# Kernel optimization log

Hardware: AMD Instinct MI355X
Metric: run time of the kernel (lower is better)

## Reference

```python
import jax, jax.numpy as jnp
import numpy as np

HIDDEN = 2048
NH = 32        # query heads
NKV = 4        # kv heads (GQA)
HD = 64        # head_dim
Q_SIZE = NH * HD      # 2048
KV_SIZE = NKV * HD    # 256
WINDOW = 1024         # sliding window size
THETA = 1000000.0
T = 2048              # tokens
SCALE = HD ** -0.5
NEG = -1e30


def setup_inputs() -> dict:
    key = jax.random.key(0)
    k1, k2, k3 = jax.random.split(key, 3)
    return {
        "positions": jnp.arange(T, dtype=jnp.int32),
        "hidden_states": jax.random.normal(k1, (T, HIDDEN), dtype=jnp.float32),
        "wqkv": jax.random.normal(k2, (HIDDEN, Q_SIZE + 2 * KV_SIZE), dtype=jnp.float32) * (HIDDEN ** -0.5),
        "wo": jax.random.normal(k3, (Q_SIZE, HIDDEN), dtype=jnp.float32) * (Q_SIZE ** -0.5),
    }


def _apply_rope(x, positions):
    # NeoX-style rotary embedding over full head_dim (rotate halves).
    half = HD // 2
    inv_freq = 1.0 / (THETA ** (jnp.arange(half, dtype=jnp.float32) / half))
    ang = positions.astype(jnp.float32)[:, None] * inv_freq[None, :]   # [T, half]
    cos = jnp.cos(ang)[:, None, :]   # [T, 1, half]
    sin = jnp.sin(ang)[:, None, :]
    x1, x2 = jnp.split(x, 2, axis=-1)
    return jnp.concatenate([x1 * cos - x2 * sin, x2 * cos + x1 * sin], axis=-1)


def reference(positions, hidden_states, wqkv, wo):
    # fused QKV projection
    qkv = hidden_states @ wqkv                          # [T, Q+2KV]
    q = qkv[:, :Q_SIZE].reshape(T, NH, HD)
    k = qkv[:, Q_SIZE:Q_SIZE + KV_SIZE].reshape(T, NKV, HD)
    v = qkv[:, Q_SIZE + KV_SIZE:].reshape(T, NKV, HD)
    # rotary embedding on q, k
    q = _apply_rope(q, positions)
    k = _apply_rope(k, positions)
    # GQA: repeat kv heads to match query heads
    group = NH // NKV
    kr = jnp.repeat(k, group, axis=1)                   # [T, NH, HD]
    vr = jnp.repeat(v, group, axis=1)
    scores = jnp.einsum('qhd,khd->hqk', q, kr) * SCALE  # [NH, T, T]
    # causal + sliding-window mask: attend to j in (i-WINDOW, i]
    i = jnp.arange(T)[:, None]
    j = jnp.arange(T)[None, :]
    mask = (j <= i) & (i - j < WINDOW)                  # [T, T]
    scores = jnp.where(mask[None, :, :], scores, NEG)
    probs = jax.nn.softmax(scores, axis=-1)
    attn = jnp.einsum('hqk,khd->qhd', probs, vr).reshape(T, Q_SIZE)
    return attn @ wo                                    # [T, HIDDEN]
```

## Files before the change

### kernel.cpp

```cpp
#include <hip/hip_runtime.h>
#include <hip/hip_bf16.h>

typedef float  f32x4  __attribute__((ext_vector_type(4)));
typedef __bf16 bf16x8 __attribute__((ext_vector_type(8)));
typedef __bf16 bf16x4 __attribute__((ext_vector_type(4)));
typedef __bf16 bf16x2 __attribute__((ext_vector_type(2)));

#define T_SEQ   2048
#define HIDDEN  2048
#define NH      32
#define NKV     4
#define HD      64
#define QSZ     2048
#define KVSZ    256
#define QKVN    2560
#define WINDOW  1024

#if __has_builtin(__builtin_amdgcn_exp2f)
#define EXPS(x) __builtin_amdgcn_exp2f(x)
#define QSCALE  0.1803368801111f
#else
#define EXPS(x) __expf(x)
#define QSCALE  0.125f
#endif

#define RAW_BARRIER()   asm volatile("s_barrier" ::: "memory")
#define WAITV(n)        asm volatile("s_waitcnt vmcnt(" #n ")" ::: "memory")

__device__ __forceinline__ void gll16(const __bf16* g, __bf16* l) {
    __builtin_amdgcn_global_load_lds(
        (const __attribute__((address_space(1))) void*)g,
        (__attribute__((address_space(3))) void*)l,
        16, 0, 0);
}

__global__ __launch_bounds__(256) void prep(const float4* __restrict__ hidden4,
                                            bf16x4* __restrict__ hidden_bf4,
                                            const float* __restrict__ wqkv,
                                            const float* __restrict__ wo,
                                            __bf16* __restrict__ wqkv_t,
                                            __bf16* __restrict__ wo_t,
                                            const int* __restrict__ pos,
                                            float2* __restrict__ ropetab) {
    __shared__ float tile[32][132];
    const int b = blockIdx.x;
    const int tid = threadIdx.x;

    if (b < 4096) {
        int id = b * 256 + tid;
        float4 v = hidden4[id];
        bf16x4 o;
        o[0] = (__bf16)v.x; o[1] = (__bf16)v.y; o[2] = (__bf16)v.z; o[3] = (__bf16)v.w;
        hidden_bf4[id] = o;
        return;
    }
    if (b < 4352) {
        int id = (b - 4096) * 256 + tid;
        int row = id >> 5, f = id & 31;
        float p = (float)pos[row];
        float ifr = exp2f((float)f * -0.62286151779138f);
        float sn, cs;
        sincosf(p * ifr, &sn, &cs);
        ropetab[id] = make_float2(cs, sn);
        return;
    }

    const float* in;
    __bf16* out;
    int Rin, Cin, bx, by;
    if (b < 5632) {
        int t = b - 4352;
        in = wqkv; out = wqkv_t; Rin = 2048; Cin = 2560;
        bx = t % 20; by = t / 20;
    } else {
        int t = b - 5632;
        in = wo; out = wo_t; Rin = 2048; Cin = 2048;
        bx = t % 16; by = t / 16;
    }
    const int ri = by * 32, ci = bx * 128;
    const int r0 = tid >> 5;
    const int c4 = tid & 31;
    #pragma unroll
    for (int i = 0; i < 4; i++) {
        float4 v = *reinterpret_cast<const float4*>(
            &in[(size_t)(ri + r0 + i * 8) * Cin + ci + c4 * 4]);
        *reinterpret_cast<float4*>(&tile[r0 + i * 8][c4 * 4]) = v;
    }
    __syncthreads();
    const int c  = tid >> 3;
    const int rb = tid & 7;
    #pragma unroll
    for (int j = 0; j < 4; j++) {
        int cc = c + j * 32;
        bf16x4 pk;
        #pragma unroll
        for (int i = 0; i < 4; i++) pk[i] = (__bf16)tile[rb * 4 + i][cc];
        *reinterpret_cast<bf16x4*>(&out[(size_t)(ci + cc) * Rin + ri + rb * 4]) = pk;
    }
}


#define GEMM_PROLOGUE(Aptr, Btptr, Kdim)                                        \
    __shared__ __align__(16) __bf16 Asm[2][64 * 64];                            \
    __shared__ __align__(16) __bf16 Bsm[2][128 * 64];                           \
    const int tid = threadIdx.x;                                                \
    const int wid = tid >> 6;                                                   \
    const int l   = tid & 63;                                                   \
    const int lg  = l >> 4;                                                     \
    const int ll  = l & 15;                                                     \
    const int swl = ll & 7;                                                     \
    const int wm  = wid >> 1, wn = wid & 1;                                     \
    const int gx   = gridDim.x;                                                 \
    const int flat = blockIdx.y * gx + blockIdx.x;                              \
    const int nwg  = gx * gridDim.y;                                            \
    const int swz  = (flat & 7) * (nwg >> 3) + (flat >> 3);                     \
    const int bm   = (swz / gx) * 64;                                           \
    const int bn   = (swz % gx) * 128;                                          \
    const __bf16* Ab = (Aptr) + (size_t)bm * (Kdim);                            \
    const __bf16* Bb = (Btptr) + (size_t)bn * (Kdim);                           \
    f32x4 acc[2][4];                                                            \
    _Pragma("unroll")                                                           \
    for (int i = 0; i < 2; i++)                                                 \
        _Pragma("unroll")                                                       \
        for (int j = 0; j < 4; j++)                                             \
            acc[i][j] = (f32x4){0.f, 0.f, 0.f, 0.f};                            \
    const int srow = tid >> 3;                                                  \
    const int sseg0 = tid & 7;

#define GEMM_STAGE(buf, k0, Kdim)                                               \
    {                                                                           \
        _Pragma("unroll")                                                       \
        for (int c = 0; c < 2; c++) {                                           \
            int row  = c * 32 + srow;                                           \
            int sseg = sseg0 ^ (row & 7);                                       \
            gll16(Ab + (size_t)row * (Kdim) + (k0) + sseg * 8,                  \
                  &Asm[buf][(c * 256 + tid) * 8]);                              \
        }                                                                       \
        _Pragma("unroll")                                                       \
        for (int c = 0; c < 4; c++) {                                           \
            int row  = c * 32 + srow;                                           \
            int sseg = sseg0 ^ (row & 7);                                       \
            gll16(Bb + (size_t)row * (Kdim) + (k0) + sseg * 8,                  \
                  &Bsm[buf][(c * 256 + tid) * 8]);                              \
        }                                                                       \
    }

#define GEMM_KLOOP(Kdim)                                                        \
    GEMM_STAGE(0, 0, Kdim)                                                      \
    int cur = 0;                                                                \
    for (int k0 = 0; k0 < (Kdim); k0 += 64) {                                   \
        RAW_BARRIER();               \
        if (k0 + 64 < (Kdim)) {                                                 \
            GEMM_STAGE(cur ^ 1, k0 + 64, Kdim)                                  \
            WAITV(6);                 \
        } else {                                                                \
            WAITV(0);                                                           \
        }                                                                       \
        RAW_BARRIER();                             \
        __builtin_amdgcn_sched_barrier(0);                                      \
        _Pragma("unroll")                                                       \
        for (int ss = 0; ss < 2; ss++) {                                        \
            bf16x8 af[2], bfr[4];                                               \
            _Pragma("unroll")                                                   \
            for (int mi = 0; mi < 2; mi++) {                                    \
                int r = wm * 32 + mi * 16 + ll;                                 \
                int u = (ss * 4 + lg) ^ swl;                                    \
                af[mi] = *reinterpret_cast<const bf16x8*>(&Asm[cur][r * 64 + u * 8]); \
            }                                                                   \
            _Pragma("unroll")                                                   \
            for (int ni = 0; ni < 4; ni++) {                                    \
                int r = wn * 64 + ni * 16 + ll;                                 \
                int u = (ss * 4 + lg) ^ swl;                                    \
                bfr[ni] = *reinterpret_cast<const bf16x8*>(&Bsm[cur][r * 64 + u * 8]); \
            }                                                                   \
            _Pragma("unroll")                                                   \
            for (int mi = 0; mi < 2; mi++)                                      \
                _Pragma("unroll")                                               \
                for (int ni = 0; ni < 4; ni++)                                  \
                    acc[mi][ni] = __builtin_amdgcn_mfma_f32_16x16x32_bf16(      \
                        af[mi], bfr[ni], acc[mi][ni], 0, 0, 0);                 \
        }                                                                       \
        cur ^= 1;                                                               \
    }

__global__ __launch_bounds__(256) void gemm_out(const __bf16* __restrict__ A,
                                                const __bf16* __restrict__ Bt,
                                                float* __restrict__ Cout,
                                                int M, int N, int K) {
    GEMM_PROLOGUE(A, Bt, K)
    GEMM_KLOOP(K)
    #pragma unroll
    for (int mi = 0; mi < 2; mi++)
        #pragma unroll
        for (int ni = 0; ni < 4; ni++)
            #pragma unroll
            for (int r = 0; r < 4; r++) {
                int row = bm + wm*32 + mi*16 + lg*4 + r;
                int col = bn + wn*64 + ni*16 + ll;
                Cout[(size_t)row * N + col] = acc[mi][ni][r];
            }
}

__global__ __launch_bounds__(256) void gemm_qkv(const __bf16* __restrict__ A,
                                                const __bf16* __restrict__ Bt,
                                                const float2* __restrict__ ropetab,
                                                __bf16* __restrict__ q,
                                                __bf16* __restrict__ k,
                                                __bf16* __restrict__ vT) {
    GEMM_PROLOGUE(A, Bt, HIDDEN)
    GEMM_KLOOP(HIDDEN)

    if (bn < QSZ + KVSZ) {
        const bool isq = (bn < QSZ);
        #pragma unroll
        for (int mi = 0; mi < 2; mi++) {
            #pragma unroll
            for (int r = 0; r < 4; r++) {
                int row = bm + wm*32 + mi*16 + lg*4 + r;
                const float2* tb = &ropetab[row * 32 + ll];
                #pragma unroll
                for (int ni = 0; ni < 2; ni++) {
                    float2 cssn = tb[ni * 16];
                    float x1 = acc[mi][ni][r], x2 = acc[mi][ni + 2][r];
                    float o1 = x1 * cssn.x - x2 * cssn.y;
                    float o2 = x2 * cssn.x + x1 * cssn.y;
                    int col = bn + wn*64 + ni*16 + ll;
                    if (isq) {
                        q[(size_t)row * QSZ + col]      = (__bf16)(o1 * QSCALE);
                        q[(size_t)row * QSZ + col + 32] = (__bf16)(o2 * QSCALE);
                    } else {
                        k[(size_t)row * KVSZ + (col - QSZ)]      = (__bf16)o1;
                        k[(size_t)row * KVSZ + (col - QSZ) + 32] = (__bf16)o2;
                    }
                }
            }
        }
    } else {
        #pragma unroll
        for (int mi = 0; mi < 2; mi++) {
            int row0 = bm + wm*32 + mi*16 + lg*4;
            #pragma unroll
            for (int ni = 0; ni < 4; ni++) {
                int d = bn + wn*64 + ni*16 + ll - (QSZ + KVSZ);
                bf16x4 pk;
                #pragma unroll
                for (int r = 0; r < 4; r++) pk[r] = (__bf16)acc[mi][ni][r];
                *reinterpret_cast<bf16x4*>(&vT[(size_t)d * T_SEQ + row0]) = pk;
            }
        }
    }
}

__global__ __launch_bounds__(512) void attn_kernel(const __bf16* __restrict__ qg,
                                                   const __bf16* __restrict__ kgl,
                                                   const __bf16* __restrict__ vTg,
                                                   __bf16* __restrict__ og) {
    const int qb  = blockIdx.x;
    const int hp  = blockIdx.y;
    const int kvh = hp >> 2;
    const int tid = threadIdx.x;
    const int wid = tid >> 6;
    const int h   = hp * 2 + (wid >> 2);
    const int l   = tid & 63;
    const int lg  = l >> 4;
    const int ll  = l & 15;
    const int i0  = qb * 64;
    const int qw  = i0 + (wid & 3) * 16;
    const int qi  = qw + ll;

    __shared__ __align__(16) __bf16 Ksm[2][64 * 64];
    __shared__ __align__(16) __bf16 VTs[2][64 * 64];

    bf16x8 qf[2];
    {
        const __bf16* qp = qg + (size_t)(qw + ll) * QSZ + h * 64 + lg * 8;
        qf[0] = *reinterpret_cast<const bf16x8*>(qp);
        qf[1] = *reinterpret_cast<const bf16x8*>(qp + 32);
    }

    f32x4 o[4];
    #pragma unroll
    for (int dn = 0; dn < 4; dn++) o[dn] = (f32x4){0.f, 0.f, 0.f, 0.f};
    float l_run = 0.f;

    int jlo = i0 - (WINDOW - 1); if (jlo < 0) jlo = 0;
    int t0v = jlo & ~63;
    int tend = i0 + 64;

    const int srow = tid >> 3;
    const int sg   = (tid & 7) ^ (srow & 7);
    const int krow = (srow & 35) | ((srow & 8) << 1) | ((srow & 4) << 1) | ((srow & 16) >> 2);
    const __bf16* kp = kgl + (size_t)krow * KVSZ + kvh * 64 + sg * 8;
    const __bf16* vp = vTg + (size_t)(kvh * 64 + srow) * T_SEQ + sg * 8;

#define ASTAGE(buf, t)                                      \
    {                                                       \
        gll16(kp + (size_t)(t) * KVSZ, &Ksm[buf][tid * 8]); \
        gll16(vp + (t),                &VTs[buf][tid * 8]); \
    }

    ASTAGE(0, t0v);

    const int swl = ll & 7;
    const int u0 = (lg ^ swl) * 8;
    const int u1 = ((4 + lg) ^ swl) * 8;

    int cur = 0;
    for (int t = t0v; t < tend; t += 64) {
        RAW_BARRIER();
        if (t + 64 < tend) {
            ASTAGE(cur ^ 1, t + 64);
            WAITV(2);
        } else {
            WAITV(0);
        }
        RAW_BARRIER();
        __builtin_amdgcn_sched_barrier(0);

        bool active = (t <= qw + 15) && (t + 63 >= qw - (WINDOW - 1));
        if (active) {
            f32x4 sT[4];
            __builtin_amdgcn_s_setprio(1);
            #pragma unroll
            for (int kt = 0; kt < 4; kt++) {
                sT[kt] = (f32x4){0.f, 0.f, 0.f, 0.f};
                bf16x8 kf0 = *reinterpret_cast<const bf16x8*>(&Ksm[cur][kt*1024 + ll*64 + u0]);
                sT[kt] = __builtin_amdgcn_mfma_f32_16x16x32_bf16(kf0, qf[0], sT[kt], 0, 0, 0);
                bf16x8 kf1 = *reinterpret_cast<const bf16x8*>(&Ksm[cur][kt*1024 + ll*64 + u1]);
                sT[kt] = __builtin_amdgcn_mfma_f32_16x16x32_bf16(kf1, qf[1], sT[kt], 0, 0, 0);
            }
            __builtin_amdgcn_s_setprio(0);

            bool full = (t + 63 <= qw) && (t >= qw + 15 - (WINDOW - 1));
            float ts = 0.f;
            if (full) {
                #pragma unroll
                for (int kt = 0; kt < 4; kt++) {
                    #pragma unroll
                    for (int r = 0; r < 4; r++) {
                        float p = EXPS(sT[kt][r]);
                        sT[kt][r] = p;
                        ts += p;
                    }
                }
            } else {
                #pragma unroll
                for (int kt = 0; kt < 4; kt++) {
                    int jb = t + ((kt & 2) << 4) + ((kt & 1) << 2) + (lg << 3);
                    #pragma unroll
                    for (int r = 0; r < 4; r++) {
                        int j = jb + r;
                        bool ok = (j <= qi) && (qi - j < WINDOW);
                        float p = ok ? EXPS(sT[kt][r]) : 0.f;
                        sT[kt][r] = p;
                        ts += p;
                    }
                }
            }
            ts += __shfl_xor(ts, 16);
            ts += __shfl_xor(ts, 32);
            l_run += ts;

            __builtin_amdgcn_s_setprio(1);
            #pragma unroll
            for (int kt2 = 0; kt2 < 2; kt2++) {
                bf16x8 pa;
                #pragma unroll
                for (int r = 0; r < 4; r++) {
                    pa[r]     = (__bf16)sT[kt2*2][r];
                    pa[r + 4] = (__bf16)sT[kt2*2 + 1][r];
                }
                int uv = kt2 ? u1 : u0;
                #pragma unroll
                for (int dn = 0; dn < 4; dn++) {
                    bf16x8 vf = *reinterpret_cast<const bf16x8*>(&VTs[cur][dn*1024 + ll*64 + uv]);
                    o[dn] = __builtin_amdgcn_mfma_f32_16x16x32_bf16(pa, vf, o[dn], 0, 0, 0);
                }
            }
            __builtin_amdgcn_s_setprio(0);
        }
        cur ^= 1;
    }
#undef ASTAGE

    float linv = 1.0f / l_run;
    float i0v = __shfl(linv, lg*4 + 0);
    float i1v = __shfl(linv, lg*4 + 1);
    float i2v = __shfl(linv, lg*4 + 2);
    float i3v = __shfl(linv, lg*4 + 3);
    #pragma unroll
    for (int dn = 0; dn < 4; dn++) {
        og[(size_t)(qw + lg*4 + 0) * QSZ + h*64 + dn*16 + ll] = (__bf16)(o[dn][0] * i0v);
        og[(size_t)(qw + lg*4 + 1) * QSZ + h*64 + dn*16 + ll] = (__bf16)(o[dn][1] * i1v);
        og[(size_t)(qw + lg*4 + 2) * QSZ + h*64 + dn*16 + ll] = (__bf16)(o[dn][2] * i2v);
        og[(size_t)(qw + lg*4 + 3) * QSZ + h*64 + dn*16 + ll] = (__bf16)(o[dn][3] * i3v);
    }
}

extern "C" void kernel_launch(void* const* d_in, const int* in_sizes, int n_in,
                              void* d_out, int out_size, void* d_ws, size_t ws_size,
                              hipStream_t stream) {
    const int*   positions = (const int*)d_in[0];
    const float* hidden    = (const float*)d_in[1];
    const float* wqkv      = (const float*)d_in[2];
    const float* wo        = (const float*)d_in[3];
    float* out = (float*)d_out;

    char* ws = (char*)d_ws;
    __bf16* hidden_bf = (__bf16*)(ws);
    __bf16* wqkv_t    = (__bf16*)(ws + 8388608);
    __bf16* wo_t      = (__bf16*)(ws + 18874368);
    __bf16* q_bf      = (__bf16*)(ws + 37748736);
    __bf16* k_bf      = (__bf16*)(ws + 46137344);
    __bf16* vT_bf     = (__bf16*)(ws + 47185920);
    __bf16* attn_bf   = (__bf16*)(ws + 48234496);
    float2* ropetab   = (float2*)(ws + 56623104);

    prep<<<dim3(6656), dim3(256), 0, stream>>>(
        (const float4*)hidden, (bf16x4*)hidden_bf, wqkv, wo,
        wqkv_t, wo_t, positions, ropetab);

    gemm_qkv<<<dim3(QKVN / 128, T_SEQ / 64), dim3(256), 0, stream>>>(
        hidden_bf, wqkv_t, ropetab, q_bf, k_bf, vT_bf);

    attn_kernel<<<dim3(T_SEQ / 64, 16), dim3(512), 0, stream>>>(
        q_bf, k_bf, vT_bf, attn_bf);

    gemm_out<<<dim3(HIDDEN / 128, T_SEQ / 64), dim3(256), 0, stream>>>(
        attn_bf, wo_t, out, T_SEQ, HIDDEN, QSZ);
}
```

Measured before the change: 106.7 us.

## Use triple-buffered LDS pipeline in output GEMM and attention kernels

Switches the output-projection GEMM and the attention K/V loop from double to triple buffering. Loads run two tiles ahead and are issued after the single per-iteration barrier, which removes one barrier per iteration. The aim is to hide more global-load latency. The cost is 50% more LDS per block in both kernels, which may reduce occupancy.

```diff
diff --git a/kernel.cpp b/kernel.cpp
--- a/kernel.cpp
+++ b/kernel.cpp
@@ -100,9 +100,7 @@
 }
 
 
-#define GEMM_PROLOGUE(Aptr, Btptr, Kdim)                                        \
-    __shared__ __align__(16) __bf16 Asm[2][64 * 64];                            \
-    __shared__ __align__(16) __bf16 Bsm[2][128 * 64];                           \
+#define GEMM_PROLOGUE_COMMON(Aptr, Btptr, Kdim)                                 \
     const int tid = threadIdx.x;                                                \
     const int wid = tid >> 6;                                                   \
     const int l   = tid & 63;                                                   \
@@ -145,50 +143,71 @@
         }                                                                       \
     }
 
-#define GEMM_KLOOP(Kdim)                                                        \
+#define GEMM_COMPUTE(bufidx)                                                    \
+    _Pragma("unroll")                                                           \
+    for (int ss = 0; ss < 2; ss++) {                                            \
+        bf16x8 af[2], bfr[4];                                                   \
+        _Pragma("unroll")                                                       \
+        for (int mi = 0; mi < 2; mi++) {                                        \
+            int r = wm * 32 + mi * 16 + ll;                                     \
+            int u = (ss * 4 + lg) ^ swl;                                        \
+            af[mi] = *reinterpret_cast<const bf16x8*>(&Asm[bufidx][r * 64 + u * 8]); \
+        }                                                                       \
+        _Pragma("unroll")                                                       \
+        for (int ni = 0; ni < 4; ni++) {                                        \
+            int r = wn * 64 + ni * 16 + ll;                                     \
+            int u = (ss * 4 + lg) ^ swl;                                        \
+            bfr[ni] = *reinterpret_cast<const bf16x8*>(&Bsm[bufidx][r * 64 + u * 8]); \
+        }                                                                       \
+        _Pragma("unroll")                                                       \
+        for (int mi = 0; mi < 2; mi++)                                          \
+            _Pragma("unroll")                                                   \
+            for (int ni = 0; ni < 4; ni++)                                      \
+                acc[mi][ni] = __builtin_amdgcn_mfma_f32_16x16x32_bf16(          \
+                    af[mi], bfr[ni], acc[mi][ni], 0, 0, 0);                     \
+    }
+
+#define GEMM_KLOOP2(Kdim)                                                       \
     GEMM_STAGE(0, 0, Kdim)                                                      \
     int cur = 0;                                                                \
     for (int k0 = 0; k0 < (Kdim); k0 += 64) {                                   \
-        RAW_BARRIER();               \
+        RAW_BARRIER();                                                          \
         if (k0 + 64 < (Kdim)) {                                                 \
             GEMM_STAGE(cur ^ 1, k0 + 64, Kdim)                                  \
-            WAITV(6);                 \
+            WAITV(6);                                                           \
         } else {                                                                \
             WAITV(0);                                                           \
         }                                                                       \
-        RAW_BARRIER();                             \
+        RAW_BARRIER();                                                          \
         __builtin_amdgcn_sched_barrier(0);                                      \
-        _Pragma("unroll")                                                       \
-        for (int ss = 0; ss < 2; ss++) {                                        \
-            bf16x8 af[2], bfr[4];                                               \
-            _Pragma("unroll")                                                   \
-            for (int mi = 0; mi < 2; mi++) {                                    \
-                int r = wm * 32 + mi * 16 + ll;                                 \
-                int u = (ss * 4 + lg) ^ swl;                                    \
-                af[mi] = *reinterpret_cast<const bf16x8*>(&Asm[cur][r * 64 + u * 8]); \
-            }                                                                   \
-            _Pragma("unroll")                                                   \
-            for (int ni = 0; ni < 4; ni++) {                                    \
-                int r = wn * 64 + ni * 16 + ll;                                 \
-                int u = (ss * 4 + lg) ^ swl;                                    \
-                bfr[ni] = *reinterpret_cast<const bf16x8*>(&Bsm[cur][r * 64 + u * 8]); \
-            }                                                                   \
-            _Pragma("unroll")                                                   \
-            for (int mi = 0; mi < 2; mi++)                                      \
-                _Pragma("unroll")                                               \
-                for (int ni = 0; ni < 4; ni++)                                  \
-                    acc[mi][ni] = __builtin_amdgcn_mfma_f32_16x16x32_bf16(      \
-                        af[mi], bfr[ni], acc[mi][ni], 0, 0, 0);                 \
-        }                                                                       \
+        GEMM_COMPUTE(cur)                                                       \
         cur ^= 1;                                                               \
+    }
+
+#define GEMM_KLOOP3(Kdim)                                                       \
+    GEMM_STAGE(0, 0, Kdim)                                                      \
+    GEMM_STAGE(1, 64, Kdim)                                                     \
+    int cur = 0;                                                                \
+    for (int k0 = 0; k0 < (Kdim); k0 += 64) {                                   \
+        if (k0 + 64 < (Kdim)) { WAITV(6); } else { WAITV(0); }                  \
+        RAW_BARRIER();                                                          \
+        __builtin_amdgcn_sched_barrier(0);                                      \
+        if (k0 + 128 < (Kdim)) {                                                \
+            int nb = cur + 2; if (nb >= 3) nb -= 3;                             \
+            GEMM_STAGE(nb, k0 + 128, Kdim)                                      \
+        }                                                                       \
+        GEMM_COMPUTE(cur)                                                       \
+        cur = (cur == 2) ? 0 : cur + 1;                                         \
     }
 
 __global__ __launch_bounds__(256) void gemm_out(const __bf16* __restrict__ A,
                                                 const __bf16* __restrict__ Bt,
                                                 float* __restrict__ Cout,
                                                 int M, int N, int K) {
-    GEMM_PROLOGUE(A, Bt, K)
-    GEMM_KLOOP(K)
+    __shared__ __align__(16) __bf16 Asm[3][64 * 64];
+    __shared__ __align__(16) __bf16 Bsm[3][128 * 64];
+    GEMM_PROLOGUE_COMMON(A, Bt, K)
+    GEMM_KLOOP3(K)
     #pragma unroll
     for (int mi = 0; mi < 2; mi++)
         #pragma unroll
@@ -207,8 +226,10 @@
                                                 __bf16* __restrict__ q,
                                                 __bf16* __restrict__ k,
                                                 __bf16* __restrict__ vT) {
-    GEMM_PROLOGUE(A, Bt, HIDDEN)
-    GEMM_KLOOP(HIDDEN)
+    __shared__ __align__(16) __bf16 Asm[2][64 * 64];
+    __shared__ __align__(16) __bf16 Bsm[2][128 * 64];
+    GEMM_PROLOGUE_COMMON(A, Bt, HIDDEN)
+    GEMM_KLOOP2(HIDDEN)
 
     if (bn < QSZ + KVSZ) {
         const bool isq = (bn < QSZ);
@@ -268,8 +289,8 @@
     const int qw  = i0 + (wid & 3) * 16;
     const int qi  = qw + ll;
 
-    __shared__ __align__(16) __bf16 Ksm[2][64 * 64];
-    __shared__ __align__(16) __bf16 VTs[2][64 * 64];
+    __shared__ __align__(16) __bf16 Ksm[3][64 * 64];
+    __shared__ __align__(16) __bf16 VTs[3][64 * 64];
 
     bf16x8 qf[2];
     {
@@ -300,6 +321,7 @@
     }
 
     ASTAGE(0, t0v);
+    if (t0v + 64 < tend) ASTAGE(1, t0v + 64);
 
     const int swl = ll & 7;
     const int u0 = (lg ^ swl) * 8;
@@ -307,15 +329,13 @@
 
     int cur = 0;
     for (int t = t0v; t < tend; t += 64) {
-        RAW_BARRIER();
-        if (t + 64 < tend) {
-            ASTAGE(cur ^ 1, t + 64);
-            WAITV(2);
-        } else {
-            WAITV(0);
-        }
+        if (t + 64 < tend) { WAITV(2); } else { WAITV(0); }
         RAW_BARRIER();
         __builtin_amdgcn_sched_barrier(0);
+        if (t + 128 < tend) {
+            int nb = cur + 2; if (nb >= 3) nb -= 3;
+            ASTAGE(nb, t + 128);
+        }
 
         bool active = (t <= qw + 15) && (t + 63 >= qw - (WINDOW - 1));
         if (active) {
@@ -379,7 +399,7 @@
             }
             __builtin_amdgcn_s_setprio(0);
         }
-        cur ^= 1;
+        cur = (cur == 2) ? 0 : cur + 1;
     }
 #undef ASTAGE
 
```

After: 106.1 us. Within noise of the previous version (-0.5%).
